# Performance work log

Measured on AMD Instinct MI355X. Metric: run time of the kernel, lower is better.

Reference implementation:

```python
import jax, jax.numpy as jnp
import numpy as np

EMB = 1024
HEADS = 16
HEAD_DIM = EMB // HEADS
EPS = 1e-5


def gelu_tanh(x):
    c = jnp.sqrt(jnp.asarray(2.0 / jnp.pi, x.dtype))
    return 0.5 * x * (1.0 + jnp.tanh(c * (x + 0.044715 * x ** 3)))


def layernorm(x, scale, shift):
    mean = jnp.mean(x, axis=-1, keepdims=True)
    var = jnp.mean((x - mean) ** 2, axis=-1, keepdims=True)  # unbiased=False
    return scale * (x - mean) / jnp.sqrt(var + EPS) + shift


def setup_inputs() -> dict:
    key = jax.random.key(0)
    ks = jax.random.split(key, 12)
    d, dff = EMB, 4 * EMB
    sd = 1.0 / np.sqrt(d)
    inp = {
        "x": jax.random.normal(ks[0], (2, 2048, d), jnp.float32),
        "Wq": jax.random.normal(ks[1], (d, d), jnp.float32) * sd,
        "Wk": jax.random.normal(ks[2], (d, d), jnp.float32) * sd,
        "Wv": jax.random.normal(ks[3], (d, d), jnp.float32) * sd,
        "Wo": jax.random.normal(ks[4], (d, d), jnp.float32) * sd,
        "bo": jnp.zeros((d,), jnp.float32),
        "W1": jax.random.normal(ks[5], (d, dff), jnp.float32) * sd,
        "b1": jnp.zeros((dff,), jnp.float32),
        "W2": jax.random.normal(ks[6], (dff, d), jnp.float32) * (1.0 / np.sqrt(dff)),
        "b2": jnp.zeros((d,), jnp.float32),
        "g1": jnp.ones((d,), jnp.float32),
        "s1": jnp.zeros((d,), jnp.float32),
        "g2": jnp.ones((d,), jnp.float32),
        "s2": jnp.zeros((d,), jnp.float32),
    }
    return inp


def attention(x, Wq, Wk, Wv, Wo, bo):
    b, s, d = x.shape
    def heads(W):
        return (x @ W).reshape(b, s, HEADS, HEAD_DIM).transpose(0, 2, 1, 3)  # b h s hd
    q, k, v = heads(Wq), heads(Wk), heads(Wv)
    scores = jnp.einsum("bhqd,bhkd->bhqk", q, k)
    causal = jnp.tril(jnp.ones((s, s), bool))
    scores = jnp.where(causal, scores, -jnp.inf)
    w = jax.nn.softmax(scores / np.sqrt(HEAD_DIM), axis=-1)
    ctx = jnp.einsum("bhqk,bhkd->bqhd", w, v).reshape(b, s, d)
    return ctx @ Wo + bo


def reference(x, Wq, Wk, Wv, Wo, bo, W1, b1, W2, b2, g1, s1, g2, s2):
    h = x + attention(layernorm(x, g1, s1), Wq, Wk, Wv, Wo, bo)
    y = layernorm(h, g2, s2)
    y = gelu_tanh(y @ W1 + b1) @ W2 + b2
    return h + y
```

## Files before the change

kernel.cpp:

```cpp
#include <hip/hip_runtime.h>
#include <hip/hip_bf16.h>
#include <stdint.h>
#include <math.h>

#define EMB   1024
#define QS    3072
#define DFF   4096
#define HEADS 16
#define HD    64
#define BATCH 2
#define SEQ   2048
#define ROWS  (BATCH * SEQ)

typedef __hip_bfloat16 bf16;
typedef short bf16x8_t __attribute__((ext_vector_type(8)));
typedef float f32x4_t __attribute__((ext_vector_type(4)));

typedef const uint32_t __attribute__((address_space(1)))* gp_t;
typedef uint32_t __attribute__((address_space(3)))* lp_t;

__device__ __forceinline__ void async_copy16(const bf16* g, short* l) {
    __builtin_amdgcn_global_load_lds((gp_t)(const void*)g, (lp_t)(void*)l, 16, 0, 0);
}

__device__ __forceinline__ void wait_lds() {
    __asm__ volatile("" ::: "memory");
    __builtin_amdgcn_s_waitcnt(0xC07F);
    __asm__ volatile("" ::: "memory");
}

__device__ __forceinline__ float gelu_f(float x) {
    float z = 0.7978845608028654f * (x + 0.044715f * x * x * x);
    float e = __builtin_amdgcn_exp2f(z * 2.885390081777927f);
    float t = 1.0f - 2.0f * __builtin_amdgcn_rcpf(e + 1.0f);
    return 0.5f * x * (1.0f + t);
}

__device__ __forceinline__ short bf16_bits(float x) {
    bf16 b = (bf16)x;
    short s;
    __builtin_memcpy(&s, &b, 2);
    return s;
}

__device__ __forceinline__ bf16x8_t load8(const bf16* p) {
    bf16x8_t v;
    __builtin_memcpy(&v, p, 16);
    return v;
}

template<int EPI, int BM, int BK>
__global__ __launch_bounds__(256) void gemm_k(
    const bf16* __restrict__ A, const bf16* __restrict__ BT,
    bf16* __restrict__ outB, float* __restrict__ outF,
    const float* __restrict__ bias, const float* __restrict__ resF,
    int N, int K, int gx)
{
    __shared__ alignas(16) short As[2][BM * BK];
    __shared__ alignas(16) short Bs[2][128 * BK];
    constexpr int AI  = BM / 32;
    constexpr int KS  = BK / 32;
    constexpr int CPR = BK / 8;
    constexpr int AIS = (BM * BK) / 2048;
    constexpr int BIS = (128 * BK) / 2048;
    const int tid  = threadIdx.x;
    const int wave = tid >> 6;
    const int lane = tid & 63;
    const int quad = lane >> 4;
    const int l16  = lane & 15;

    const int nb  = (int)gridDim.x;
    const int q8  = nb >> 3;
    const int lid = ((int)blockIdx.x & 7) * q8 + ((int)blockIdx.x >> 3);
    const int bx = lid % gx;
    const int by = lid / gx;
    const int m0 = by * BM;
    const int n0 = bx * 128;
    const int wm = (wave >> 1) * (BM / 2);
    const int wn = (wave & 1) * 64;

    const bf16* Ag[AIS]; int aoff[AIS];
    const bf16* Bg[BIS]; int boff[BIS];
    #pragma unroll
    for (int i = 0; i < AIS; i++) {
        const int c = i * 256 + tid;
        const int row = c / CPR, pc = c % CPR;
        const int lch = (BK == 64) ? (pc ^ (row & 7)) : (pc ^ ((row >> 1) & 3));
        Ag[i]   = A + (size_t)(m0 + row) * K + lch * 8;
        aoff[i] = (i * 256 + wave * 64) * 8;
    }
    #pragma unroll
    for (int i = 0; i < BIS; i++) {
        const int c = i * 256 + tid;
        const int row = c / CPR, pc = c % CPR;
        const int lch = (BK == 64) ? (pc ^ (row & 7)) : (pc ^ ((row >> 1) & 3));
        Bg[i]   = BT + (size_t)(n0 + row) * K + lch * 8;
        boff[i] = (i * 256 + wave * 64) * 8;
    }

    f32x4_t acc[AI][4] = {};

    #pragma unroll
    for (int i = 0; i < AIS; i++) async_copy16(Ag[i], &As[0][aoff[i]]);
    #pragma unroll
    for (int i = 0; i < BIS; i++) async_copy16(Bg[i], &Bs[0][boff[i]]);
    __syncthreads();

    int cur = 0;
    for (int k0 = 0; k0 < K; k0 += BK) {
        const int kn = k0 + BK;
        if (kn < K) {
            #pragma unroll
            for (int i = 0; i < AIS; i++) async_copy16(Ag[i] + kn, &As[cur ^ 1][aoff[i]]);
            #pragma unroll
            for (int i = 0; i < BIS; i++) async_copy16(Bg[i] + kn, &Bs[cur ^ 1][boff[i]]);
        }
        bf16x8_t a[AI][KS], b[4][KS];
        #pragma unroll
        for (int ks = 0; ks < KS; ks++) {
            #pragma unroll
            for (int i = 0; i < AI; i++) {
                const int r = wm + i * 16 + l16;
                const int s = ks * 4 + quad;
                const int ph = (BK == 64) ? (s ^ (r & 7)) : (s ^ ((r >> 1) & 3));
                a[i][ks] = *(const bf16x8_t*)&As[cur][r * BK + ph * 8];
            }
            #pragma unroll
            for (int j = 0; j < 4; j++) {
                const int r = wn + j * 16 + l16;
                const int s = ks * 4 + quad;
                const int ph = (BK == 64) ? (s ^ (r & 7)) : (s ^ ((r >> 1) & 3));
                b[j][ks] = *(const bf16x8_t*)&Bs[cur][r * BK + ph * 8];
            }
        }
        #pragma unroll
        for (int ks = 0; ks < KS; ks++)
            #pragma unroll
            for (int i = 0; i < AI; i++)
                #pragma unroll
                for (int j = 0; j < 4; j++)
                    acc[i][j] = __builtin_amdgcn_mfma_f32_16x16x32_bf16(
                        a[i][ks], b[j][ks], acc[i][j], 0, 0, 0);
        __syncthreads();
        cur ^= 1;
    }

    #pragma unroll
    for (int j = 0; j < 4; j++) {
        const int col = n0 + wn + j * 16 + l16;
        float bv = 0.0f;
        if constexpr (EPI != 0) bv = bias[col];
        #pragma unroll
        for (int i = 0; i < AI; i++) {
            #pragma unroll
            for (int r = 0; r < 4; r++) {
                const int row = m0 + wm + i * 16 + quad * 4 + r;
                float v = acc[i][j][r] + bv;
                if constexpr (EPI == 1 || EPI == 3) {
                    v += resF[(size_t)row * N + col];
                    outF[(size_t)row * N + col] = v;
                } else if constexpr (EPI == 2) {
                    outB[(size_t)row * N + col] = (bf16)gelu_f(v);
                } else {
                    outB[(size_t)row * N + col] = (bf16)v;
                }
            }
        }
    }
}

__global__ __launch_bounds__(256) void ln_k(
    const float* __restrict__ x, const float* __restrict__ g,
    const float* __restrict__ s, bf16* __restrict__ out)
{
    const int row = blockIdx.x;
    const int t = threadIdx.x;
    const size_t base = (size_t)row * EMB + t * 4;
    float v[4];
    #pragma unroll
    for (int e = 0; e < 4; e++) v[e] = x[base + e];
    float sum = v[0] + v[1] + v[2] + v[3];
    float sq  = v[0]*v[0] + v[1]*v[1] + v[2]*v[2] + v[3]*v[3];
    #pragma unroll
    for (int o = 1; o < 64; o <<= 1) {
        sum += __shfl_xor(sum, o);
        sq  += __shfl_xor(sq, o);
    }
    __shared__ float ssum[4], ssq[4];
    const int wave = t >> 6;
    if ((t & 63) == 0) { ssum[wave] = sum; ssq[wave] = sq; }
    __syncthreads();
    sum = ssum[0] + ssum[1] + ssum[2] + ssum[3];
    sq  = ssq[0] + ssq[1] + ssq[2] + ssq[3];
    const float mean = sum * (1.0f / EMB);
    const float var  = sq * (1.0f / EMB) - mean * mean;
    const float rstd = rsqrtf(var + 1e-5f);
    #pragma unroll
    for (int e = 0; e < 4; e++)
        out[base + e] = (bf16)(g[t * 4 + e] * (v[e] - mean) * rstd + s[t * 4 + e]);
}

__global__ __launch_bounds__(256) void transpose_k(
    const float* __restrict__ src, bf16* __restrict__ dst, int R, int C)
{
    __shared__ bf16 tile[64][65];
    const int tx = threadIdx.x, ty = threadIdx.y;
    const int r0 = blockIdx.y * 64, c0 = blockIdx.x * 64;
    #pragma unroll
    for (int i = 0; i < 16; i++) {
        int r = ty + i * 4;
        tile[r][tx] = (bf16)src[(size_t)(r0 + r) * C + c0 + tx];
    }
    __syncthreads();
    #pragma unroll
    for (int i = 0; i < 16; i++) {
        int c = ty + i * 4;
        dst[(size_t)(c0 + c) * R + r0 + tx] = tile[tx][c];
    }
}

__global__ __launch_bounds__(256) void transpose3_k(
    const float* __restrict__ s0, const float* __restrict__ s1,
    const float* __restrict__ s2, bf16* __restrict__ dst, int R, int C)
{
    __shared__ bf16 tile[64][65];
    const float* src = blockIdx.z == 0 ? s0 : (blockIdx.z == 1 ? s1 : s2);
    bf16* d = dst + (size_t)blockIdx.z * R * C;
    const int tx = threadIdx.x, ty = threadIdx.y;
    const int r0 = blockIdx.y * 64, c0 = blockIdx.x * 64;
    #pragma unroll
    for (int i = 0; i < 16; i++) {
        int r = ty + i * 4;
        tile[r][tx] = (bf16)src[(size_t)(r0 + r) * C + c0 + tx];
    }
    __syncthreads();
    #pragma unroll
    for (int i = 0; i < 16; i++) {
        int c = ty + i * 4;
        d[(size_t)(c0 + c) * R + r0 + tx] = tile[tx][c];
    }
}

__global__ __launch_bounds__(256) void transpose_v_k(
    const bf16* __restrict__ src, bf16* __restrict__ dst)
{
    __shared__ bf16 tile[64][65];
    const int tx = threadIdx.x, ty = threadIdx.y;
    const int r0 = blockIdx.y * 64, c0 = blockIdx.x * 64;
    const size_t so = (size_t)blockIdx.z * SEQ * QS;
    const size_t do_ = (size_t)blockIdx.z * EMB * SEQ;
    #pragma unroll
    for (int i = 0; i < 16; i++) {
        int r = ty + i * 4;
        tile[r][tx] = src[so + (size_t)(r0 + r) * QS + c0 + tx];
    }
    __syncthreads();
    #pragma unroll
    for (int i = 0; i < 16; i++) {
        int c = ty + i * 4;
        dst[do_ + (size_t)(c0 + c) * SEQ + r0 + tx] = tile[tx][c];
    }
}

__global__ __launch_bounds__(256) void attn_k(
    const bf16* __restrict__ qkv, const bf16* __restrict__ vt,
    bf16* __restrict__ ctx)
{
    __shared__ alignas(16) short Ks[2][64 * 64];
    __shared__ alignas(16) short Vs[2][64 * 64];
    __shared__ alignas(16) short P[4][16 * 40];
    const int tid = threadIdx.x;
    const int wv = tid >> 6;
    const int lane = tid & 63;
    const int quad = lane >> 4, l16 = lane & 15;

    const int fid = (int)blockIdx.x;
    const int lid = (fid & 7) * 64 + (fid >> 3);
    const int p = lid & 15;
    const int h = (lid >> 4) & 15;
    const int b = lid >> 8;
    const size_t rowBase = (size_t)b * SEQ;

    const bf16* kcol  = qkv + 1024 + rowBase * QS + h * HD;
    const bf16* vbase = vt + (size_t)(b * HEADS + h) * HD * SEQ;

    int krw[2], kgc[2];
    #pragma unroll
    for (int i = 0; i < 2; i++) {
        const int c = i * 256 + tid;
        krw[i] = c >> 3;
        kgc[i] = (c & 7) ^ (krw[i] & 7);
    }
    const int ldsOff[2] = { (0 * 256 + wv * 64) * 8, (1 * 256 + wv * 64) * 8 };

    constexpr float SC = 0.125f * 1.44269504088896f;

    #pragma unroll
    for (int i = 0; i < 2; i++) {
        async_copy16(kcol + (size_t)krw[i] * QS + kgc[i] * 8, &Ks[0][ldsOff[i]]);
        async_copy16(vbase + (size_t)krw[i] * SEQ + kgc[i] * 8, &Vs[0][ldsOff[i]]);
    }
    __syncthreads();

    int cur = 0;
    #pragma unroll
    for (int g = 0; g < 2; g++) {
        const int chunk = g ? p : (31 - p);
        const int NK = chunk + 1;
        const int qb = chunk * 64 + wv * 16;

        bf16x8_t aq[2];
        #pragma unroll
        for (int s2 = 0; s2 < 2; s2++)
            aq[s2] = load8(&qkv[(rowBase + qb + l16) * QS + h * HD + s2 * 32 + quad * 8]);

        f32x4_t O[4] = {};
        float l_p[4] = {};

        for (int kb = 0; kb < NK; ++kb) {
            const int kbase = kb * 64;
            const bool more = (kb + 1 < NK) || (g == 0);
            if (more) {
                const int nb = (kb + 1 < NK) ? kbase + 64 : 0;
                #pragma unroll
                for (int i = 0; i < 2; i++) {
                    async_copy16(kcol + (size_t)(nb + krw[i]) * QS + kgc[i] * 8,
                                 &Ks[cur ^ 1][ldsOff[i]]);
                    async_copy16(vbase + (size_t)krw[i] * SEQ + nb + kgc[i] * 8,
                                 &Vs[cur ^ 1][ldsOff[i]]);
                }
            }
            bf16x8_t ck[4][2];
            #pragma unroll
            for (int nt = 0; nt < 4; nt++) {
                const int kr = nt * 16 + l16;
                #pragma unroll
                for (int s2 = 0; s2 < 2; s2++)
                    ck[nt][s2] = *(const bf16x8_t*)
                        &Ks[cur][kr * 64 + (((s2 * 4 + quad) ^ (kr & 7)) << 3)];
            }
            f32x4_t sc[4] = {};
            __builtin_amdgcn_s_setprio(1);
            #pragma unroll
            for (int nt = 0; nt < 4; nt++)
                #pragma unroll
                for (int s2 = 0; s2 < 2; s2++)
                    sc[nt] = __builtin_amdgcn_mfma_f32_16x16x32_bf16(
                        aq[s2], ck[nt][s2], sc[nt], 0, 0, 0);
            __builtin_amdgcn_s_setprio(0);

            short* Pw = P[wv];
            const bool full = (kbase + 63 <= qb);
            #pragma unroll
            for (int hf = 0; hf < 2; hf++) {
                bf16x8_t cv[4];
                #pragma unroll
                for (int c = 0; c < 4; c++) {
                    const int vr = c * 16 + l16;
                    cv[c] = *(const bf16x8_t*)
                        &Vs[cur][vr * 64 + (((hf * 4 + quad) ^ (vr & 7)) << 3)];
                }
                if (full) {
                    #pragma unroll
                    for (int nt2 = 0; nt2 < 2; nt2++) {
                        const int nt = hf * 2 + nt2;
                        #pragma unroll
                        for (int r = 0; r < 4; r++) {
                            const float pe = __builtin_amdgcn_exp2f(sc[nt][r] * SC);
                            l_p[r] += pe;
                            Pw[(quad * 4 + r) * 40 + nt2 * 16 + l16] = bf16_bits(pe);
                        }
                    }
                } else {
                    #pragma unroll
                    for (int nt2 = 0; nt2 < 2; nt2++) {
                        const int nt = hf * 2 + nt2;
                        const int kk = kbase + nt * 16 + l16;
                        #pragma unroll
                        for (int r = 0; r < 4; r++) {
                            const int qg = qb + quad * 4 + r;
                            float s = sc[nt][r] * SC;
                            if (kk > qg) s = -1e30f;
                            const float pe = __builtin_amdgcn_exp2f(s);
                            l_p[r] += pe;
                            Pw[(quad * 4 + r) * 40 + nt2 * 16 + l16] = bf16_bits(pe);
                        }
                    }
                }
                wait_lds();
                bf16x8_t pa = *(const bf16x8_t*)&Pw[l16 * 40 + quad * 8];
                __builtin_amdgcn_s_setprio(1);
                #pragma unroll
                for (int c = 0; c < 4; c++)
                    O[c] = __builtin_amdgcn_mfma_f32_16x16x32_bf16(pa, cv[c], O[c], 0, 0, 0);
                __builtin_amdgcn_s_setprio(0);
            }
            __syncthreads();
            cur ^= 1;
        }

        #pragma unroll
        for (int r = 0; r < 4; r++) {
            float l = l_p[r];
            l += __shfl_xor(l, 1);
            l += __shfl_xor(l, 2);
            l += __shfl_xor(l, 4);
            l += __shfl_xor(l, 8);
            const float inv = 1.0f / l;
            #pragma unroll
            for (int c = 0; c < 4; c++)
                ctx[(rowBase + qb + quad * 4 + r) * EMB + h * HD + c * 16 + l16]
                    = (bf16)(O[c][r] * inv);
        }
    }
}

extern "C" void kernel_launch(void* const* d_in, const int* in_sizes, int n_in,
                              void* d_out, int out_size, void* d_ws, size_t ws_size,
                              hipStream_t stream) {
    const float* X  = (const float*)d_in[0];
    const float* Wq = (const float*)d_in[1];
    const float* Wk = (const float*)d_in[2];
    const float* Wv = (const float*)d_in[3];
    const float* Wo = (const float*)d_in[4];
    const float* bo = (const float*)d_in[5];
    const float* W1 = (const float*)d_in[6];
    const float* b1 = (const float*)d_in[7];
    const float* W2 = (const float*)d_in[8];
    const float* b2 = (const float*)d_in[9];
    const float* g1 = (const float*)d_in[10];
    const float* s1 = (const float*)d_in[11];
    const float* g2 = (const float*)d_in[12];
    const float* s2 = (const float*)d_in[13];
    float* out = (float*)d_out;

    char* ws = (char*)d_ws;
    const size_t MB = 1024 * 1024;
    bf16*  lnbuf = (bf16*)(ws + 0);
    bf16*  qkv   = (bf16*)(ws + 8 * MB);
    bf16*  vtb   = (bf16*)(ws + 32 * MB);
    bf16*  ctx   = (bf16*)(ws + 40 * MB);
    float* hbuf  = (float*)(ws + 48 * MB);
    bf16*  WqT   = (bf16*)(ws + 64 * MB);
    bf16*  WoT   = (bf16*)(ws + 70 * MB);
    bf16*  ffn1  = (bf16*)(ws + 8 * MB);
    bf16*  W1T   = (bf16*)(ws + 40 * MB);
    bf16*  W2T   = (bf16*)(ws + 64 * MB);

    const dim3 tb(64, 4);
    transpose3_k<<<dim3(16, 16, 3), tb, 0, stream>>>(Wq, Wk, Wv, WqT, EMB, EMB);
    transpose_k<<<dim3(16, 16, 1), tb, 0, stream>>>(Wo, WoT, EMB, EMB);

    ln_k<<<ROWS, 256, 0, stream>>>(X, g1, s1, lnbuf);

    gemm_k<0, 128, 32><<<768, 256, 0, stream>>>(
        lnbuf, WqT, qkv, nullptr, nullptr, nullptr, QS, EMB, 24);

    transpose_v_k<<<dim3(16, 32, BATCH), tb, 0, stream>>>(qkv + 2048, vtb);

    attn_k<<<512, 256, 0, stream>>>(qkv, vtb, ctx);

    gemm_k<1, 64, 64><<<512, 256, 0, stream>>>(
        ctx, WoT, nullptr, hbuf, bo, X, EMB, EMB, 8);

    transpose_k<<<dim3(64, 16, 1), tb, 0, stream>>>(W1, W1T, EMB, DFF);
    transpose_k<<<dim3(16, 64, 1), tb, 0, stream>>>(W2, W2T, DFF, EMB);

    ln_k<<<ROWS, 256, 0, stream>>>(hbuf, g2, s2, lnbuf);

    gemm_k<2, 128, 32><<<1024, 256, 0, stream>>>(
        lnbuf, W1T, ffn1, nullptr, b1, nullptr, DFF, EMB, 32);

    gemm_k<3, 64, 64><<<512, 256, 0, stream>>>(
        ffn1, W2T, nullptr, out, b2, hbuf, EMB, DFF, 8);
}
```

Before: 347.8 us.

## Fuse paired causal query chunks in attention and tile GEMM blocks per XCD

The attention kernel previously handled its two query chunks (31-p and p) one after the other, streaming K/V tiles twice. It now processes both chunks in a single pass over the K/V tiles, so each tile loaded into LDS serves both chunks until the shorter one finishes, and the wrap-around prefetch is gone. The block-to-(head,batch) mapping is also changed so each XCD holds specific heads, which aims to improve L2 locality. GEMM block mapping now assigns each XCD a rectangular sub-grid of tiles (gxs by rows) for better L2 reuse of A and B. In exchange the attention kernel uses more registers for two sets of accumulators, which may lower occupancy.

```diff
diff --git a/kernel.cpp b/kernel.cpp
--- a/kernel.cpp
+++ b/kernel.cpp
@@ -54,7 +54,7 @@
     const bf16* __restrict__ A, const bf16* __restrict__ BT,
     bf16* __restrict__ outB, float* __restrict__ outF,
     const float* __restrict__ bias, const float* __restrict__ resF,
-    int N, int K, int gx)
+    int N, int K, int gxs, int cxn)
 {
     __shared__ alignas(16) short As[2][BM * BK];
     __shared__ alignas(16) short Bs[2][128 * BK];
@@ -69,11 +69,12 @@
     const int quad = lane >> 4;
     const int l16  = lane & 15;
 
-    const int nb  = (int)gridDim.x;
-    const int q8  = nb >> 3;
-    const int lid = ((int)blockIdx.x & 7) * q8 + ((int)blockIdx.x >> 3);
-    const int bx = lid % gx;
-    const int by = lid / gx;
+    const int q8  = (int)gridDim.x >> 3;
+    const int xcd = (int)blockIdx.x & 7;
+    const int l2  = (int)blockIdx.x >> 3;
+    const int cx  = xcd % cxn, cy = xcd / cxn;
+    const int bx  = cx * gxs + l2 % gxs;
+    const int by  = cy * (q8 / gxs) + l2 / gxs;
     const int m0 = by * BM;
     const int n0 = bx * 128;
     const int wm = (wave >> 1) * (BM / 2);
@@ -268,21 +269,38 @@
 {
     __shared__ alignas(16) short Ks[2][64 * 64];
     __shared__ alignas(16) short Vs[2][64 * 64];
-    __shared__ alignas(16) short P[4][16 * 40];
+    __shared__ alignas(16) short P[4][2][16 * 40];
     const int tid = threadIdx.x;
     const int wv = tid >> 6;
     const int lane = tid & 63;
     const int quad = lane >> 4, l16 = lane & 15;
 
     const int fid = (int)blockIdx.x;
-    const int lid = (fid & 7) * 64 + (fid >> 3);
-    const int p = lid & 15;
-    const int h = (lid >> 4) & 15;
-    const int b = lid >> 8;
+    const int xcd = fid & 7, n = fid >> 3;
+    const int praw = n & 15;
+    const int p = (n >= 32) ? (15 - praw) : praw;
+    const int h = xcd + 8 * ((n >> 4) & 1);
+    const int b = n >> 5;
     const size_t rowBase = (size_t)b * SEQ;
+
+    const int cA = 31 - p, cB = p;
+    const int NKA = cA + 1;
+    const int NKB = cB + 1;
+    const int qbA = cA * 64 + wv * 16;
+    const int qbB = cB * 64 + wv * 16;
 
     const bf16* kcol  = qkv + 1024 + rowBase * QS + h * HD;
     const bf16* vbase = vt + (size_t)(b * HEADS + h) * HD * SEQ;
+
+    bf16x8_t aqA[2], aqB[2];
+    #pragma unroll
+    for (int s2 = 0; s2 < 2; s2++) {
+        aqA[s2] = load8(&qkv[(rowBase + qbA + l16) * QS + h * HD + s2 * 32 + quad * 8]);
+        aqB[s2] = load8(&qkv[(rowBase + qbB + l16) * QS + h * HD + s2 * 32 + quad * 8]);
+    }
+
+    f32x4_t OA[4] = {}, OB[4] = {};
+    float lA[4] = {}, lB[4] = {};
 
     int krw[2], kgc[2];
     #pragma unroll
@@ -303,71 +321,68 @@
     __syncthreads();
 
     int cur = 0;
-    #pragma unroll
-    for (int g = 0; g < 2; g++) {
-        const int chunk = g ? p : (31 - p);
-        const int NK = chunk + 1;
-        const int qb = chunk * 64 + wv * 16;
-
-        bf16x8_t aq[2];
-        #pragma unroll
-        for (int s2 = 0; s2 < 2; s2++)
-            aq[s2] = load8(&qkv[(rowBase + qb + l16) * QS + h * HD + s2 * 32 + quad * 8]);
-
-        f32x4_t O[4] = {};
-        float l_p[4] = {};
-
-        for (int kb = 0; kb < NK; ++kb) {
-            const int kbase = kb * 64;
-            const bool more = (kb + 1 < NK) || (g == 0);
-            if (more) {
-                const int nb = (kb + 1 < NK) ? kbase + 64 : 0;
-                #pragma unroll
-                for (int i = 0; i < 2; i++) {
-                    async_copy16(kcol + (size_t)(nb + krw[i]) * QS + kgc[i] * 8,
-                                 &Ks[cur ^ 1][ldsOff[i]]);
-                    async_copy16(vbase + (size_t)krw[i] * SEQ + nb + kgc[i] * 8,
-                                 &Vs[cur ^ 1][ldsOff[i]]);
-                }
-            }
-            bf16x8_t ck[4][2];
-            #pragma unroll
-            for (int nt = 0; nt < 4; nt++) {
-                const int kr = nt * 16 + l16;
-                #pragma unroll
-                for (int s2 = 0; s2 < 2; s2++)
-                    ck[nt][s2] = *(const bf16x8_t*)
-                        &Ks[cur][kr * 64 + (((s2 * 4 + quad) ^ (kr & 7)) << 3)];
-            }
-            f32x4_t sc[4] = {};
-            __builtin_amdgcn_s_setprio(1);
+    for (int kb = 0; kb < NKA; ++kb) {
+        const int kbase = kb * 64;
+        if (kb + 1 < NKA) {
+            const int nb = kbase + 64;
+            #pragma unroll
+            for (int i = 0; i < 2; i++) {
+                async_copy16(kcol + (size_t)(nb + krw[i]) * QS + kgc[i] * 8,
+                             &Ks[cur ^ 1][ldsOff[i]]);
+                async_copy16(vbase + (size_t)krw[i] * SEQ + nb + kgc[i] * 8,
+                             &Vs[cur ^ 1][ldsOff[i]]);
+            }
+        }
+        const bool doB = (kb < NKB);
+
+        bf16x8_t ck[4][2];
+        #pragma unroll
+        for (int nt = 0; nt < 4; nt++) {
+            const int kr = nt * 16 + l16;
+            #pragma unroll
+            for (int s2 = 0; s2 < 2; s2++)
+                ck[nt][s2] = *(const bf16x8_t*)
+                    &Ks[cur][kr * 64 + (((s2 * 4 + quad) ^ (kr & 7)) << 3)];
+        }
+        f32x4_t scA[4] = {}, scB[4] = {};
+        __builtin_amdgcn_s_setprio(1);
+        #pragma unroll
+        for (int nt = 0; nt < 4; nt++)
+            #pragma unroll
+            for (int s2 = 0; s2 < 2; s2++)
+                scA[nt] = __builtin_amdgcn_mfma_f32_16x16x32_bf16(
+                    aqA[s2], ck[nt][s2], scA[nt], 0, 0, 0);
+        if (doB) {
             #pragma unroll
             for (int nt = 0; nt < 4; nt++)
                 #pragma unroll
                 for (int s2 = 0; s2 < 2; s2++)
-                    sc[nt] = __builtin_amdgcn_mfma_f32_16x16x32_bf16(
-                        aq[s2], ck[nt][s2], sc[nt], 0, 0, 0);
-            __builtin_amdgcn_s_setprio(0);
-
-            short* Pw = P[wv];
-            const bool full = (kbase + 63 <= qb);
-            #pragma unroll
-            for (int hf = 0; hf < 2; hf++) {
-                bf16x8_t cv[4];
-                #pragma unroll
-                for (int c = 0; c < 4; c++) {
-                    const int vr = c * 16 + l16;
-                    cv[c] = *(const bf16x8_t*)
-                        &Vs[cur][vr * 64 + (((hf * 4 + quad) ^ (vr & 7)) << 3)];
-                }
-                if (full) {
+                    scB[nt] = __builtin_amdgcn_mfma_f32_16x16x32_bf16(
+                        aqB[s2], ck[nt][s2], scB[nt], 0, 0, 0);
+        }
+        __builtin_amdgcn_s_setprio(0);
+
+        const bool fullA = (kbase + 63 <= qbA);
+        const bool fullB = (kbase + 63 <= qbB);
+        #pragma unroll
+        for (int hf = 0; hf < 2; hf++) {
+            bf16x8_t cv[4];
+            #pragma unroll
+            for (int c = 0; c < 4; c++) {
+                const int vr = c * 16 + l16;
+                cv[c] = *(const bf16x8_t*)
+                    &Vs[cur][vr * 64 + (((hf * 4 + quad) ^ (vr & 7)) << 3)];
+            }
+            {
+                short* Pw = P[wv][0];
+                if (fullA) {
                     #pragma unroll
                     for (int nt2 = 0; nt2 < 2; nt2++) {
                         const int nt = hf * 2 + nt2;
                         #pragma unroll
                         for (int r = 0; r < 4; r++) {
-                            const float pe = __builtin_amdgcn_exp2f(sc[nt][r] * SC);
-                            l_p[r] += pe;
+                            const float pe = __builtin_amdgcn_exp2f(scA[nt][r] * SC);
+                            lA[r] += pe;
                             Pw[(quad * 4 + r) * 40 + nt2 * 16 + l16] = bf16_bits(pe);
                         }
                     }
@@ -378,40 +393,89 @@
                         const int kk = kbase + nt * 16 + l16;
                         #pragma unroll
                         for (int r = 0; r < 4; r++) {
-                            const int qg = qb + quad * 4 + r;
-                            float s = sc[nt][r] * SC;
+                            const int qg = qbA + quad * 4 + r;
+                            float s = scA[nt][r] * SC;
                             if (kk > qg) s = -1e30f;
                             const float pe = __builtin_amdgcn_exp2f(s);
-                            l_p[r] += pe;
+                            lA[r] += pe;
                             Pw[(quad * 4 + r) * 40 + nt2 * 16 + l16] = bf16_bits(pe);
                         }
                     }
                 }
-                wait_lds();
-                bf16x8_t pa = *(const bf16x8_t*)&Pw[l16 * 40 + quad * 8];
-                __builtin_amdgcn_s_setprio(1);
+            }
+            if (doB) {
+                short* Pw = P[wv][1];
+                if (fullB) {
+                    #pragma unroll
+                    for (int nt2 = 0; nt2 < 2; nt2++) {
+                        const int nt = hf * 2 + nt2;
+                        #pragma unroll
+                        for (int r = 0; r < 4; r++) {
+                            const float pe = __builtin_amdgcn_exp2f(scB[nt][r] * SC);
+                            lB[r] += pe;
+                            Pw[(quad * 4 + r) * 40 + nt2 * 16 + l16] = bf16_bits(pe);
+                        }
+                    }
+                } else {
+                    #pragma unroll
+                    for (int nt2 = 0; nt2 < 2; nt2++) {
+                        const int nt = hf * 2 + nt2;
+                        const int kk = kbase + nt * 16 + l16;
+                        #pragma unroll
+                        for (int r = 0; r < 4; r++) {
+                            const int qg = qbB + quad * 4 + r;
+                            float s = scB[nt][r] * SC;
+                            if (kk > qg) s = -1e30f;
+                            const float pe = __builtin_amdgcn_exp2f(s);
+                            lB[r] += pe;
+                            Pw[(quad * 4 + r) * 40 + nt2 * 16 + l16] = bf16_bits(pe);
+                        }
+                    }
+                }
+            }
+            wait_lds();
+            bf16x8_t paA = *(const bf16x8_t*)&P[wv][0][l16 * 40 + quad * 8];
+            __builtin_amdgcn_s_setprio(1);
+            #pragma unroll
+            for (int c = 0; c < 4; c++)
+                OA[c] = __builtin_amdgcn_mfma_f32_16x16x32_bf16(paA, cv[c], OA[c], 0, 0, 0);
+            if (doB) {
+                bf16x8_t paB = *(const bf16x8_t*)&P[wv][1][l16 * 40 + quad * 8];
                 #pragma unroll
                 for (int c = 0; c < 4; c++)
-                    O[c] = __builtin_amdgcn_mfma_f32_16x16x32_bf16(pa, cv[c], O[c], 0, 0, 0);
-                __builtin_amdgcn_s_setprio(0);
-            }
-            __syncthreads();
-            cur ^= 1;
-        }
-
-        #pragma unroll
-        for (int r = 0; r < 4; r++) {
-            float l = l_p[r];
-            l += __shfl_xor(l, 1);
-            l += __shfl_xor(l, 2);
-            l += __shfl_xor(l, 4);
-            l += __shfl_xor(l, 8);
-            const float inv = 1.0f / l;
-            #pragma unroll
-            for (int c = 0; c < 4; c++)
-                ctx[(rowBase + qb + quad * 4 + r) * EMB + h * HD + c * 16 + l16]
-                    = (bf16)(O[c][r] * inv);
-        }
+                    OB[c] = __builtin_amdgcn_mfma_f32_16x16x32_bf16(paB, cv[c], OB[c], 0, 0, 0);
+            }
+            __builtin_amdgcn_s_setprio(0);
+        }
+        __syncthreads();
+        cur ^= 1;
+    }
+
+    #pragma unroll
+    for (int r = 0; r < 4; r++) {
+        float l = lA[r];
+        l += __shfl_xor(l, 1);
+        l += __shfl_xor(l, 2);
+        l += __shfl_xor(l, 4);
+        l += __shfl_xor(l, 8);
+        const float inv = 1.0f / l;
+        #pragma unroll
+        for (int c = 0; c < 4; c++)
+            ctx[(rowBase + qbA + quad * 4 + r) * EMB + h * HD + c * 16 + l16]
+                = (bf16)(OA[c][r] * inv);
+    }
+    #pragma unroll
+    for (int r = 0; r < 4; r++) {
+        float l = lB[r];
+        l += __shfl_xor(l, 1);
+        l += __shfl_xor(l, 2);
+        l += __shfl_xor(l, 4);
+        l += __shfl_xor(l, 8);
+        const float inv = 1.0f / l;
+        #pragma unroll
+        for (int c = 0; c < 4; c++)
+            ctx[(rowBase + qbB + quad * 4 + r) * EMB + h * HD + c * 16 + l16]
+                = (bf16)(OB[c][r] * inv);
     }
 }
 
@@ -454,14 +518,14 @@
     ln_k<<<ROWS, 256, 0, stream>>>(X, g1, s1, lnbuf);
 
     gemm_k<0, 128, 32><<<768, 256, 0, stream>>>(
-        lnbuf, WqT, qkv, nullptr, nullptr, nullptr, QS, EMB, 24);
+        lnbuf, WqT, qkv, nullptr, nullptr, nullptr, QS, EMB, 12, 2);
 
     transpose_v_k<<<dim3(16, 32, BATCH), tb, 0, stream>>>(qkv + 2048, vtb);
 
     attn_k<<<512, 256, 0, stream>>>(qkv, vtb, ctx);
 
     gemm_k<1, 64, 64><<<512, 256, 0, stream>>>(
-        ctx, WoT, nullptr, hbuf, bo, X, EMB, EMB, 8);
+        ctx, WoT, nullptr, hbuf, bo, X, EMB, EMB, 8, 1);
 
     transpose_k<<<dim3(64, 16, 1), tb, 0, stream>>>(W1, W1T, EMB, DFF);
     transpose_k<<<dim3(16, 64, 1), tb, 0, stream>>>(W2, W2T, DFF, EMB);
@@ -469,8 +533,8 @@
     ln_k<<<ROWS, 256, 0, stream>>>(hbuf, g2, s2, lnbuf);
 
     gemm_k<2, 128, 32><<<1024, 256, 0, stream>>>(
-        lnbuf, W1T, ffn1, nullptr, b1, nullptr, DFF, EMB, 32);
+        lnbuf, W1T, ffn1, nullptr, b1, nullptr, DFF, EMB, 16, 2);
 
     gemm_k<3, 64, 64><<<512, 256, 0, stream>>>(
-        ffn1, W2T, nullptr, out, b2, hbuf, EMB, DFF, 8);
-}
+        ffn1, W2T, nullptr, out, b2, hbuf, EMB, DFF, 8, 1);
+}
```

New measurement: 353.7 us. No clear change (+1.7%).
